# Optimization experiments

Measured on AMD Instinct MI355X. Metric: run time of the kernel, lower is better.

Reference implementation:

```python
import jax, jax.numpy as jnp
import numpy as np

B, T, C = 4, 1024, 768
H, HS = 12, 64           # num_heads, head_size
VD = 2 * HS              # value dim per head


def setup_inputs() -> dict:
    key = jax.random.key(0)
    ks = jax.random.split(key, 16)
    s = 0.02
    inp = {
        "x": jax.random.normal(ks[0], (B, T, C), jnp.float32),
        "Wq1": jax.random.normal(ks[1], (H, C, HS), jnp.float32) * s,
        "Wk1": jax.random.normal(ks[2], (H, C, HS), jnp.float32) * s,
        "Wq2": jax.random.normal(ks[3], (H, C, HS), jnp.float32) * s,
        "Wk2": jax.random.normal(ks[4], (H, C, HS), jnp.float32) * s,
        "Wv": jax.random.normal(ks[5], (H, C, VD), jnp.float32) * s,
        "lq1": jax.random.normal(ks[6], (H, HS), jnp.float32) * 0.1,
        "lk1": jax.random.normal(ks[7], (H, HS), jnp.float32) * 0.1,
        "lq2": jax.random.normal(ks[8], (H, HS), jnp.float32) * 0.1,
        "lk2": jax.random.normal(ks[9], (H, HS), jnp.float32) * 0.1,
        "gn_w": jnp.ones((H * VD,), jnp.float32),
        "gn_b": jnp.zeros((H * VD,), jnp.float32),
        "Wp": jax.random.normal(ks[10], (C, H * VD), jnp.float32) * s,
        "bp": jnp.zeros((C,), jnp.float32),
        "layer_idx": 3,
    }
    return inp


def _diff_attn(x, Wq1, Wk1, Wq2, Wk2, Wv, lq1, lk1, lq2, lk2,
               gn_w, gn_b, Wp, bp, layer_idx):
    Bc, Tc, _ = x.shape
    scale = 1.0 / jnp.sqrt(jnp.float32(HS))
    # per-head projections: [B,H,T,HS]
    q1 = jnp.einsum('btc,hcd->bhtd', x, Wq1)
    k1 = jnp.einsum('btc,hcd->bhtd', x, Wk1)
    q2 = jnp.einsum('btc,hcd->bhtd', x, Wq2)
    k2 = jnp.einsum('btc,hcd->bhtd', x, Wk2)
    v = jnp.einsum('btc,hce->bhte', x, Wv)           # [B,H,T,2HS]
    mask = jnp.tril(jnp.ones((Tc, Tc), bool))         # causal
    neg = jnp.float32(-jnp.inf)
    a1 = jnp.einsum('bhtd,bhsd->bhts', q1, k1) * scale
    a2 = jnp.einsum('bhtd,bhsd->bhts', q2, k2) * scale
    a1 = jax.nn.softmax(jnp.where(mask, a1, neg), axis=-1)
    a2 = jax.nn.softmax(jnp.where(mask, a2, neg), axis=-1)
    # dynamic lambda init, per get_lambda
    li = jnp.float32(layer_idx)
    dyn = 0.8 - 0.6 * jnp.exp(-0.3 * (li - 1.0))
    lam = jnp.mean(jnp.exp(lq1 * lk1) - jnp.exp(lq2 * lk2) + dyn, axis=-1)  # [H]
    diff = a1 - lam[None, :, None, None] * a2
    out = jnp.einsum('bhts,bhse->bhte', diff, v)      # [B,H,T,2HS]
    out = out.transpose(0, 2, 1, 3).reshape(Bc, Tc, H * VD)
    # GroupLayerNorm == full layernorm over last dim (unbiased=False var)
    mu = out.mean(-1, keepdims=True)
    var = jnp.mean((out - mu) ** 2, axis=-1, keepdims=True)
    out = (out - mu) / jnp.sqrt(var + 1e-5) * gn_w + gn_b
    out = out * 0.2  # (1 - lambda_init_buffer=0.8), buffer never updated
    return out @ Wp.T + bp


def reference(x, Wq1, Wk1, Wq2, Wk2, Wv, lq1, lk1, lq2, lk2,
              gn_w, gn_b, Wp, bp, layer_idx):
    return _diff_attn(x, Wq1, Wk1, Wq2, Wk2, Wv, lq1, lk1, lq2, lk2,
                      gn_w, gn_b, Wp, bp, layer_idx)
```

## Files before the change

### kernel.cpp

```cpp
#include <hip/hip_runtime.h>
#include <hip/hip_bf16.h>

#define Bc   4
#define Tc   1024
#define Cc   768
#define Hc   12
#define HSc  64
#define VDc  128
#define NQKV 4608
#define YLD  3072
#define NROWS 4096
#define HVD  1536

#define Q1OFF 0
#define K1OFF 768
#define Q2OFF 1536
#define K2OFF 2304

typedef __bf16 bf16x8 __attribute__((ext_vector_type(8)));
typedef float f32x4 __attribute__((ext_vector_type(4)));
typedef unsigned int u32x4 __attribute__((ext_vector_type(4)));

#define EXP2SCALE 0.18033688011112042f

static __device__ __forceinline__ float bf2f(unsigned short s) {
    return __uint_as_float(((unsigned int)s) << 16);
}
static __device__ __forceinline__ unsigned short f2bf(float f) {
    unsigned int u = __float_as_uint(f);
    unsigned int r = (u + 0x7FFFu + ((u >> 16) & 1u)) >> 16;
    return (unsigned short)r;
}
static __device__ __forceinline__ unsigned int pack2bf(float lo, float hi) {
    unsigned int a = (__float_as_uint(lo) + 0x8000u) >> 16;
    unsigned int b = (__float_as_uint(hi) + 0x8000u) & 0xFFFF0000u;
    return a | b;
}
static __device__ __forceinline__ float fast_exp2(float x) {
    float r;
    asm("v_exp_f32 %0, %1" : "=v"(r) : "v"(x));
    return r;
}

static __device__ __forceinline__ void load16_lds(const void* g, void* l) {
    __builtin_amdgcn_global_load_lds(
        (const __attribute__((address_space(1))) void*)g,
        (__attribute__((address_space(3))) void*)l, 16, 0, 0);
}

__global__ __launch_bounds__(256) void cast_bf16(
    const float* __restrict__ src, unsigned short* __restrict__ dst)
{
    int i = blockIdx.x * 256 + threadIdx.x;
    float4 v = *(const float4*)(src + (size_t)i * 4);
    ushort4 u;
    u.x = f2bf(v.x); u.y = f2bf(v.y); u.z = f2bf(v.z); u.w = f2bf(v.w);
    *(ushort4*)(dst + (size_t)i * 4) = u;
}

__global__ __launch_bounds__(256) void trans_w(
    const float* __restrict__ Wq1, const float* __restrict__ Wk1,
    const float* __restrict__ Wq2, const float* __restrict__ Wk2,
    const float* __restrict__ Wv, unsigned short* __restrict__ WcatT)
{
    __shared__ float tile[64][65];
    int tid = threadIdx.x;
    int t = blockIdx.x;
    int kt = t % 12, nt = t / 12;
    int k0 = kt * 64, n0 = nt * 64;
    const float* src;
    int stride;
    if (n0 < 3072) {
        int which = n0 / 768, m = n0 - which * 768, h = m >> 6;
        const float* W = (which == 0) ? Wq1 : (which == 1) ? Wk1 : (which == 2) ? Wq2 : Wk2;
        src = W + ((size_t)h * 768 + k0) * 64;
        stride = 64;
    } else {
        int rel = n0 - 3072, h = rel >> 7, e0 = rel & 127;
        src = Wv + ((size_t)h * 768 + k0) * 128 + e0;
        stride = 128;
    }
    for (int i = tid; i < 4096; i += 256) {
        int kl = i >> 6, dl = i & 63;
        tile[dl][kl] = src[(size_t)kl * stride + dl];
    }
    __syncthreads();
    for (int i = tid; i < 4096; i += 256) {
        int nl = i >> 6, kl = i & 63;
        WcatT[(size_t)(n0 + nl) * 768 + k0 + kl] = f2bf(tile[nl][kl]);
    }
}

__global__ __launch_bounds__(64) void lambda_kernel(
    const float* __restrict__ lq1, const float* __restrict__ lk1,
    const float* __restrict__ lq2, const float* __restrict__ lk2,
    const int* __restrict__ layer_idx, float* __restrict__ lam)
{
    int h = blockIdx.x, l = threadIdx.x;
    float li = (float)layer_idx[0];
    float dyn = 0.8f - 0.6f * expf(-0.3f * (li - 1.0f));
    int i = h * HSc + l;
    float v = expf(lq1[i] * lk1[i]) - expf(lq2[i] * lk2[i]) + dyn;
    #pragma unroll
    for (int off = 32; off; off >>= 1) v += __shfl_xor(v, off);
    if (l == 0) lam[h] = v * (1.0f / 64.0f);
}

template<int TN, int KD, int LDC, bool OUT_BIAS, bool SPLITV>
__global__ __launch_bounds__(256) void gemm_mfma(
    const unsigned short* __restrict__ A, const unsigned short* __restrict__ Bt,
    unsigned short* __restrict__ Cb, float* __restrict__ Cf,
    const float* __restrict__ bias, unsigned short* __restrict__ VtOut)
{
    constexpr int BN = TN * 32;
    constexpr int JB = TN / 2;
    __shared__ unsigned short As[128 * 64];
    __shared__ unsigned short Bs[BN * 64];
    int tid = threadIdx.x, lane = tid & 63, w = tid >> 6;
    int wm = w >> 1, wn = w & 1;
    int m0 = blockIdx.y * 128, n0 = blockIdx.x * BN;

    int lr = lane >> 2, lq = lane & 3;
    const unsigned short* gA[2];
    const unsigned short* gB[JB];
    #pragma unroll
    for (int j = 0; j < 2; ++j) {
        int row = w * 32 + j * 16 + lr;
        int qg = lq ^ ((row >> 1) & 3);
        gA[j] = A + (size_t)(m0 + row) * KD + qg * 8;
    }
    #pragma unroll
    for (int j = 0; j < JB; ++j) {
        int row = w * (JB * 16) + j * 16 + lr;
        int qg = lq ^ ((row >> 1) & 3);
        gB[j] = Bt + (size_t)(n0 + row) * KD + qg * 8;
    }

    int rr = lane & 15, qd = lane >> 4;
    const unsigned short* aAddr[4];
    const unsigned short* bAddr[TN];
    #pragma unroll
    for (int i = 0; i < 4; ++i) {
        int row = wm * 64 + i * 16 + rr;
        int qs = qd ^ ((row >> 1) & 3);
        aAddr[i] = As + row * 32 + qs * 8;
    }
    #pragma unroll
    for (int t = 0; t < TN; ++t) {
        int row = wn * (TN * 16) + t * 16 + rr;
        int qs = qd ^ ((row >> 1) & 3);
        bAddr[t] = Bs + row * 32 + qs * 8;
    }

    f32x4 acc[4][TN];
    #pragma unroll
    for (int i = 0; i < 4; ++i)
        #pragma unroll
        for (int t = 0; t < TN; ++t) acc[i][t] = {0.f, 0.f, 0.f, 0.f};

    for (int k = 0; k < KD / 64; ++k) {
        __syncthreads();
        load16_lds(gA[0], As + (w * 2 + 0) * 512);
        load16_lds(gA[1], As + (w * 2 + 1) * 512);
        load16_lds(gA[0] + 32, As + 4096 + (w * 2 + 0) * 512);
        load16_lds(gA[1] + 32, As + 4096 + (w * 2 + 1) * 512);
        #pragma unroll
        for (int j = 0; j < JB; ++j) {
            load16_lds(gB[j], Bs + (w * JB + j) * 512);
            load16_lds(gB[j] + 32, Bs + BN * 32 + (w * JB + j) * 512);
        }
        gA[0] += 64; gA[1] += 64;
        #pragma unroll
        for (int j = 0; j < JB; ++j) gB[j] += 64;
        __syncthreads();

        bf16x8 af0[4], af1[4], bf0[TN], bf1[TN];
        #pragma unroll
        for (int i = 0; i < 4; ++i) {
            af0[i] = *(const bf16x8*)aAddr[i];
            af1[i] = *(const bf16x8*)(aAddr[i] + 4096);
        }
        #pragma unroll
        for (int t = 0; t < TN; ++t) {
            bf0[t] = *(const bf16x8*)bAddr[t];
            bf1[t] = *(const bf16x8*)(bAddr[t] + BN * 32);
        }
        #pragma unroll
        for (int i = 0; i < 4; ++i)
            #pragma unroll
            for (int t = 0; t < TN; ++t) {
                acc[i][t] = __builtin_amdgcn_mfma_f32_16x16x32_bf16(af0[i], bf0[t], acc[i][t], 0, 0, 0);
                acc[i][t] = __builtin_amdgcn_mfma_f32_16x16x32_bf16(af1[i], bf1[t], acc[i][t], 0, 0, 0);
            }
    }

    #pragma unroll
    for (int t = 0; t < TN; ++t) {
        int col = n0 + wn * (TN * 16) + t * 16 + rr;
        if (SPLITV && col >= 3072) {
            int rel = col - 3072, hh = rel >> 7, e = rel & 127;
            #pragma unroll
            for (int i = 0; i < 4; ++i) {
                int row0 = m0 + wm * 64 + i * 16 + qd * 4;
                int b = row0 >> 10, tt = row0 & 1023;
                ushort4 pk;
                pk.x = f2bf(acc[i][t][0]); pk.y = f2bf(acc[i][t][1]);
                pk.z = f2bf(acc[i][t][2]); pk.w = f2bf(acc[i][t][3]);
                *(ushort4*)&VtOut[(size_t)((b * Hc + hh) * 128 + e) * 1024 + tt] = pk;
            }
        } else {
            float bv = OUT_BIAS ? bias[col] : 0.f;
            #pragma unroll
            for (int i = 0; i < 4; ++i) {
                #pragma unroll
                for (int r = 0; r < 4; ++r) {
                    int row = m0 + wm * 64 + i * 16 + qd * 4 + r;
                    if (OUT_BIAS)
                        Cf[(size_t)row * LDC + col] = acc[i][t][r] + bv;
                    else
                        Cb[(size_t)row * LDC + col] = f2bf(acc[i][t][r]);
                }
            }
        }
    }
}

__global__ __launch_bounds__(256) void diff_attn_mfma(
    const unsigned short* __restrict__ Y, const unsigned short* __restrict__ Vt,
    const float* __restrict__ lam_buf, unsigned short* __restrict__ attn)
{
    __shared__ __align__(16) unsigned short KVring[2 * 16384];

    int bh = blockIdx.x;
    int b = bh / Hc, h = bh - b * Hc;
    int g = 15 - (int)blockIdx.y;
    int tid = threadIdx.x, lane = tid & 63, wv = tid >> 6;
    int cl = lane & 15, qd = lane >> 4;
    float lamv = lam_buf[h];
    size_t rowbase = (size_t)(b * Tc) * YLD;
    const int hq = h * HSc;
    const unsigned short* VtB = Vt + ((size_t)bh << 17);
    const f32x4 zero4 = {0.f, 0.f, 0.f, 0.f};

    int sub = wv & 1;
    int off8[8];
    int dstoff;
    if (wv < 2) {
        int ksrow = lane >> 3;
        int ksch  = (lane & 7) ^ ksrow;
        #pragma unroll
        for (int j = 0; j < 8; ++j) {
            int moff = (j < 4) ? K1OFF : K2OFF;
            off8[j] = ((j & 3) * 8 + ksrow) * YLD + moff + hq + ksch * 8;
        }
        dstoff = 0;
    } else {
        int vsel = lane >> 2;
        int vsch = (lane & 3) ^ ((vsel >> 1) & 3);
        #pragma unroll
        for (int s = 0; s < 8; ++s)
            off8[s] = (s * 16 + vsel) * 1024 + vsch * 8;
        dstoff = 8192;
    }

    auto stage = [&](int i, int slot) {
        int kt = 2 * i + sub;
        char* base = (char*)KVring + slot * 32768 + sub * 16384 + dstoff;
        const unsigned short* g0 = (wv < 2)
            ? (Y + rowbase + (size_t)(kt * 32) * YLD)
            : (VtB + kt * 32);
        #pragma unroll
        for (int j = 0; j < 8; ++j)
            load16_lds(g0 + off8[j], base + j * 1024);
    };

    int kfo[2][4], vfo[8];
    #pragma unroll
    for (int c = 0; c < 2; ++c) {
        int row = c * 16 + cl;
        #pragma unroll
        for (int j = 0; j < 4; ++j)
            kfo[c][j] = (j >> 1) * 4096 + row * 128 +
                        ((((j & 1) * 4 + qd) ^ (row & 7)) << 4);
    }
    #pragma unroll
    for (int ec = 0; ec < 8; ++ec) {
        int e = ec * 16 + cl;
        vfo[ec] = 8192 + e * 64 + ((qd ^ ((e >> 1) & 3)) << 4);
    }

    int idxA = ((32 * (qd & 1)) + cl) * 4;
    int idxB = idxA + 64;
    bool loHalf = (qd < 2);

    int qrow = g * 64 + wv * 16;

    stage(0, 0);

    size_t qoff = rowbase + (size_t)(qrow + cl) * YLD;
    bf16x8 q1a = *(const bf16x8*)(Y + qoff + Q1OFF + hq + qd * 8);
    bf16x8 q1b = *(const bf16x8*)(Y + qoff + Q1OFF + hq + 32 + qd * 8);
    bf16x8 q2a = *(const bf16x8*)(Y + qoff + Q2OFF + hq + qd * 8);
    bf16x8 q2b = *(const bf16x8*)(Y + qoff + Q2OFF + hq + 32 + qd * 8);

    f32x4 O1[8], O2[8];
    #pragma unroll
    for (int ec = 0; ec < 8; ++ec) { O1[ec] = zero4; O2[ec] = zero4; }
    float l1s = 0.f, l2s = 0.f;

    auto transform = [&](f32x4 S1[2], f32x4 S2[2], int kt,
                         bf16x8& pa1o, bf16x8& pa2o) {
        if (kt * 32 + 31 > qrow) {
            #pragma unroll
            for (int c = 0; c < 2; ++c) {
                int lim = qrow + cl - kt * 32 - c * 16 - qd * 4;
                #pragma unroll
                for (int r = 0; r < 4; ++r) {
                    if (r > lim) { S1[c][r] = -1e30f; S2[c][r] = -1e30f; }
                }
            }
        }
        float p1v[2][4], p2v[2][4];
        #pragma unroll
        for (int c = 0; c < 2; ++c) {
            #pragma unroll
            for (int r = 0; r < 4; ++r) {
                p1v[c][r] = fast_exp2(S1[c][r] * EXP2SCALE);
                p2v[c][r] = fast_exp2(S2[c][r] * EXP2SCALE);
                l1s += p1v[c][r];
                l2s += p2v[c][r];
            }
        }
        unsigned int s1m[2][2], s2m[2][2];
        #pragma unroll
        for (int c = 0; c < 2; ++c) {
            s1m[c][0] = pack2bf(p1v[c][0], p1v[c][1]);
            s1m[c][1] = pack2bf(p1v[c][2], p1v[c][3]);
            s2m[c][0] = pack2bf(p2v[c][0], p2v[c][1]);
            s2m[c][1] = pack2bf(p2v[c][2], p2v[c][3]);
        }
        u32x4 U1, U2;
        {
            int a00 = __builtin_amdgcn_ds_bpermute(idxA, (int)s1m[0][0]);
            int a10 = __builtin_amdgcn_ds_bpermute(idxA, (int)s1m[1][0]);
            int a01 = __builtin_amdgcn_ds_bpermute(idxA, (int)s1m[0][1]);
            int a11 = __builtin_amdgcn_ds_bpermute(idxA, (int)s1m[1][1]);
            int b00 = __builtin_amdgcn_ds_bpermute(idxB, (int)s1m[0][0]);
            int b10 = __builtin_amdgcn_ds_bpermute(idxB, (int)s1m[1][0]);
            int b01 = __builtin_amdgcn_ds_bpermute(idxB, (int)s1m[0][1]);
            int b11 = __builtin_amdgcn_ds_bpermute(idxB, (int)s1m[1][1]);
            U1[0] = (unsigned)(loHalf ? a00 : a10);
            U1[1] = (unsigned)(loHalf ? a01 : a11);
            U1[2] = (unsigned)(loHalf ? b00 : b10);
            U1[3] = (unsigned)(loHalf ? b01 : b11);
        }
        {
            int a00 = __builtin_amdgcn_ds_bpermute(idxA, (int)s2m[0][0]);
            int a10 = __builtin_amdgcn_ds_bpermute(idxA, (int)s2m[1][0]);
            int a01 = __builtin_amdgcn_ds_bpermute(idxA, (int)s2m[0][1]);
            int a11 = __builtin_amdgcn_ds_bpermute(idxA, (int)s2m[1][1]);
            int b00 = __builtin_amdgcn_ds_bpermute(idxB, (int)s2m[0][0]);
            int b10 = __builtin_amdgcn_ds_bpermute(idxB, (int)s2m[1][0]);
            int b01 = __builtin_amdgcn_ds_bpermute(idxB, (int)s2m[0][1]);
            int b11 = __builtin_amdgcn_ds_bpermute(idxB, (int)s2m[1][1]);
            U2[0] = (unsigned)(loHalf ? a00 : a10);
            U2[1] = (unsigned)(loHalf ? a01 : a11);
            U2[2] = (unsigned)(loHalf ? b00 : b10);
            U2[3] = (unsigned)(loHalf ? b01 : b11);
        }
        pa1o = __builtin_bit_cast(bf16x8, U1);
        pa2o = __builtin_bit_cast(bf16x8, U2);
    };

    int NI = g + 1;
    for (int i = 0; i < NI; ++i) {
        asm volatile("s_waitcnt vmcnt(0)\n\ts_barrier" ::: "memory");
        const char* kbA = (const char*)KVring + (i & 1) * 32768;
        const char* kbB = kbA + 16384;
        if (i + 1 < NI) stage(i + 1, (i + 1) & 1);

        bf16x8 kfA[2][4], kfB[2][4];
        #pragma unroll
        for (int c = 0; c < 2; ++c)
            #pragma unroll
            for (int j = 0; j < 4; ++j) {
                kfA[c][j] = *(const bf16x8*)(kbA + kfo[c][j]);
                kfB[c][j] = *(const bf16x8*)(kbB + kfo[c][j]);
            }
        bf16x8 vfA[8];
        #pragma unroll
        for (int ec = 0; ec < 8; ++ec)
            vfA[ec] = *(const bf16x8*)(kbA + vfo[ec]);

        f32x4 S1A[2], S2A[2], S1B[2], S2B[2];
        #pragma unroll
        for (int c = 0; c < 2; ++c) {
            S1A[c] = zero4; S2A[c] = zero4; S1B[c] = zero4; S2B[c] = zero4;
        }
        #pragma unroll
        for (int c = 0; c < 2; ++c) {
            S1A[c] = __builtin_amdgcn_mfma_f32_16x16x32_bf16(kfA[c][0], q1a, S1A[c], 0, 0, 0);
            S1A[c] = __builtin_amdgcn_mfma_f32_16x16x32_bf16(kfA[c][1], q1b, S1A[c], 0, 0, 0);
            S2A[c] = __builtin_amdgcn_mfma_f32_16x16x32_bf16(kfA[c][2], q2a, S2A[c], 0, 0, 0);
            S2A[c] = __builtin_amdgcn_mfma_f32_16x16x32_bf16(kfA[c][3], q2b, S2A[c], 0, 0, 0);
            S1B[c] = __builtin_amdgcn_mfma_f32_16x16x32_bf16(kfB[c][0], q1a, S1B[c], 0, 0, 0);
            S1B[c] = __builtin_amdgcn_mfma_f32_16x16x32_bf16(kfB[c][1], q1b, S1B[c], 0, 0, 0);
            S2B[c] = __builtin_amdgcn_mfma_f32_16x16x32_bf16(kfB[c][2], q2a, S2B[c], 0, 0, 0);
            S2B[c] = __builtin_amdgcn_mfma_f32_16x16x32_bf16(kfB[c][3], q2b, S2B[c], 0, 0, 0);
        }

        bf16x8 pa1A, pa2A, pa1B, pa2B;
        transform(S1A, S2A, 2 * i, pa1A, pa2A);
        bf16x8 vfB[8];
        #pragma unroll
        for (int ec = 0; ec < 8; ++ec)
            vfB[ec] = *(const bf16x8*)(kbB + vfo[ec]);
        transform(S1B, S2B, 2 * i + 1, pa1B, pa2B);

        #pragma unroll
        for (int ec = 0; ec < 8; ++ec) {
            O1[ec] = __builtin_amdgcn_mfma_f32_16x16x32_bf16(pa1A, vfA[ec], O1[ec], 0, 0, 0);
            O2[ec] = __builtin_amdgcn_mfma_f32_16x16x32_bf16(pa2A, vfA[ec], O2[ec], 0, 0, 0);
        }
        #pragma unroll
        for (int ec = 0; ec < 8; ++ec) {
            O1[ec] = __builtin_amdgcn_mfma_f32_16x16x32_bf16(pa1B, vfB[ec], O1[ec], 0, 0, 0);
            O2[ec] = __builtin_amdgcn_mfma_f32_16x16x32_bf16(pa2B, vfB[ec], O2[ec], 0, 0, 0);
        }
    }

    l1s += __shfl_xor(l1s, 16); l1s += __shfl_xor(l1s, 32);
    l2s += __shfl_xor(l2s, 16); l2s += __shfl_xor(l2s, 32);
    float w1[4], w2[4];
    #pragma unroll
    for (int r = 0; r < 4; ++r) {
        float d1 = __shfl(l1s, qd * 4 + r);
        float d2 = __shfl(l2s, qd * 4 + r);
        w1[r] = 1.0f / d1;
        w2[r] = lamv / d2;
    }
    #pragma unroll
    for (int ec = 0; ec < 8; ++ec) {
        #pragma unroll
        for (int r = 0; r < 4; ++r) {
            size_t row = (size_t)(b * Tc + qrow + qd * 4 + r);
            attn[row * HVD + h * VDc + ec * 16 + cl] =
                f2bf(O1[ec][r] * w1[r] - O2[ec][r] * w2[r]);
        }
    }
}

__global__ __launch_bounds__(128) void ln_inplace(
    unsigned short* __restrict__ attn,
    const float* __restrict__ gnw, const float* __restrict__ gnb)
{
    int row = blockIdx.x, tid = threadIdx.x;
    unsigned short* p = attn + (size_t)row * HVD;
    float v[12];
    float s = 0.f, sq = 0.f;
    #pragma unroll
    for (int j = 0; j < 3; ++j) {
        int g = tid + j * 128;
        ushort4 u = *(const ushort4*)(p + g * 4);
        float x0 = bf2f(u.x), x1 = bf2f(u.y), x2 = bf2f(u.z), x3 = bf2f(u.w);
        v[j * 4 + 0] = x0; v[j * 4 + 1] = x1; v[j * 4 + 2] = x2; v[j * 4 + 3] = x3;
        s += x0 + x1 + x2 + x3;
        sq = fmaf(x0, x0, sq); sq = fmaf(x1, x1, sq);
        sq = fmaf(x2, x2, sq); sq = fmaf(x3, x3, sq);
    }
    #pragma unroll
    for (int off = 32; off; off >>= 1) { s += __shfl_xor(s, off); sq += __shfl_xor(sq, off); }
    __shared__ float ss[2], sqs[2];
    if ((tid & 63) == 0) { ss[tid >> 6] = s; sqs[tid >> 6] = sq; }
    __syncthreads();
    float S = ss[0] + ss[1], Q = sqs[0] + sqs[1];
    float mu = S * (1.0f / HVD);
    float rstd = rsqrtf(Q * (1.0f / HVD) - mu * mu + 1e-5f);
    #pragma unroll
    for (int j = 0; j < 3; ++j) {
        int g = tid + j * 128;
        float4 gw = *(const float4*)(gnw + g * 4);
        float4 gb = *(const float4*)(gnb + g * 4);
        ushort4 o;
        o.x = f2bf(((v[j * 4 + 0] - mu) * rstd * gw.x + gb.x) * 0.2f);
        o.y = f2bf(((v[j * 4 + 1] - mu) * rstd * gw.y + gb.y) * 0.2f);
        o.z = f2bf(((v[j * 4 + 2] - mu) * rstd * gw.z + gb.z) * 0.2f);
        o.w = f2bf(((v[j * 4 + 3] - mu) * rstd * gw.w + gb.w) * 0.2f);
        *(ushort4*)(p + g * 4) = o;
    }
}

extern "C" void kernel_launch(void* const* d_in, const int* in_sizes, int n_in,
                              void* d_out, int out_size, void* d_ws, size_t ws_size,
                              hipStream_t stream)
{
    const float* x   = (const float*)d_in[0];
    const float* Wq1 = (const float*)d_in[1];
    const float* Wk1 = (const float*)d_in[2];
    const float* Wq2 = (const float*)d_in[3];
    const float* Wk2 = (const float*)d_in[4];
    const float* Wv  = (const float*)d_in[5];
    const float* lq1 = (const float*)d_in[6];
    const float* lk1 = (const float*)d_in[7];
    const float* lq2 = (const float*)d_in[8];
    const float* lk2 = (const float*)d_in[9];
    const float* gnw = (const float*)d_in[10];
    const float* gnb = (const float*)d_in[11];
    const float* Wp  = (const float*)d_in[12];
    const float* bp  = (const float*)d_in[13];
    const int*   lidx = (const int*)d_in[14];
    float* out = (float*)d_out;

    char* w = (char*)d_ws;
    unsigned short* WcatT = (unsigned short*)(w);
    unsigned short* Xb    = (unsigned short*)(w + 7077888);
    unsigned short* Y     = (unsigned short*)(w + 13369344);
    unsigned short* VtW   = (unsigned short*)(w + 38535168);
    unsigned short* attn  = (unsigned short*)(w + 51118080);
    unsigned short* Wpb   = (unsigned short*)(w + 63700992);
    float* lam            = (float*)(w + 66060288);

    cast_bf16<<<dim3(NROWS * Cc / 1024), 256, 0, stream>>>(x, Xb);
    cast_bf16<<<dim3(Cc * HVD / 1024), 256, 0, stream>>>(Wp, Wpb);
    trans_w<<<dim3(72 * 12), 256, 0, stream>>>(Wq1, Wk1, Wq2, Wk2, Wv, WcatT);
    lambda_kernel<<<dim3(Hc), 64, 0, stream>>>(lq1, lk1, lq2, lk2, lidx, lam);
    gemm_mfma<4, 768, YLD, false, true><<<dim3(NQKV / 128, NROWS / 128), 256, 0, stream>>>(
        Xb, WcatT, Y, nullptr, nullptr, VtW);
    diff_attn_mfma<<<dim3(Bc * Hc, 16), 256, 0, stream>>>(Y, VtW, lam, attn);
    ln_inplace<<<dim3(NROWS), 128, 0, stream>>>(attn, gnw, gnb);
    gemm_mfma<2, HVD, Cc, true, false><<<dim3(Cc / 64, NROWS / 128), 256, 0, stream>>>(
        attn, Wpb, nullptr, out, bp, nullptr);
}
```

Measured before the change: 240.5 us.

## Merge prep kernels and remap GEMM blocks for XCD-local L2 reuse

Folds the two fp32-to-bf16 casts and the lambda computation into a single prep kernel, removing two launches. Both GEMMs switch to a 1D grid with a block-index swizzle: the low 3 bits pick an XCD, and each XCD is given 4 consecutive M tiles, so tiles that share A rows stay in one XCD's L2. This aims to cut launch overhead and L2 misses. It depends on blocks being dispatched round-robin across the 8 XCDs, and the index arithmetic only matches the current 32 M tiles.

```diff
diff --git a/kernel.cpp b/kernel.cpp
--- a/kernel.cpp
+++ b/kernel.cpp
@@ -48,14 +48,37 @@
         (__attribute__((address_space(3))) void*)l, 16, 0, 0);
 }
 
-__global__ __launch_bounds__(256) void cast_bf16(
-    const float* __restrict__ src, unsigned short* __restrict__ dst)
+__global__ __launch_bounds__(256) void prep(
+    const float* __restrict__ x, const float* __restrict__ Wp,
+    const float* __restrict__ lq1, const float* __restrict__ lk1,
+    const float* __restrict__ lq2, const float* __restrict__ lk2,
+    const int* __restrict__ layer_idx,
+    unsigned short* __restrict__ Xb, unsigned short* __restrict__ Wpb,
+    float* __restrict__ lam)
 {
-    int i = blockIdx.x * 256 + threadIdx.x;
-    float4 v = *(const float4*)(src + (size_t)i * 4);
-    ushort4 u;
-    u.x = f2bf(v.x); u.y = f2bf(v.y); u.z = f2bf(v.z); u.w = f2bf(v.w);
-    *(ushort4*)(dst + (size_t)i * 4) = u;
+    int bid = blockIdx.x, tid = threadIdx.x;
+    if (bid < 3072) {
+        size_t i = (size_t)bid * 256 + tid;
+        float4 v = *(const float4*)(x + i * 4);
+        ushort4 u;
+        u.x = f2bf(v.x); u.y = f2bf(v.y); u.z = f2bf(v.z); u.w = f2bf(v.w);
+        *(ushort4*)(Xb + i * 4) = u;
+    } else if (bid < 4224) {
+        size_t i = (size_t)(bid - 3072) * 256 + tid;
+        float4 v = *(const float4*)(Wp + i * 4);
+        ushort4 u;
+        u.x = f2bf(v.x); u.y = f2bf(v.y); u.z = f2bf(v.z); u.w = f2bf(v.w);
+        *(ushort4*)(Wpb + i * 4) = u;
+    } else if (tid < 64) {
+        int h = bid - 4224, l = tid;
+        float li = (float)layer_idx[0];
+        float dyn = 0.8f - 0.6f * expf(-0.3f * (li - 1.0f));
+        int i = h * HSc + l;
+        float v = expf(lq1[i] * lk1[i]) - expf(lq2[i] * lk2[i]) + dyn;
+        #pragma unroll
+        for (int off = 32; off; off >>= 1) v += __shfl_xor(v, off);
+        if (l == 0) lam[h] = v * (1.0f / 64.0f);
+    }
 }
 
 __global__ __launch_bounds__(256) void trans_w(
@@ -91,21 +114,6 @@
     }
 }
 
-__global__ __launch_bounds__(64) void lambda_kernel(
-    const float* __restrict__ lq1, const float* __restrict__ lk1,
-    const float* __restrict__ lq2, const float* __restrict__ lk2,
-    const int* __restrict__ layer_idx, float* __restrict__ lam)
-{
-    int h = blockIdx.x, l = threadIdx.x;
-    float li = (float)layer_idx[0];
-    float dyn = 0.8f - 0.6f * expf(-0.3f * (li - 1.0f));
-    int i = h * HSc + l;
-    float v = expf(lq1[i] * lk1[i]) - expf(lq2[i] * lk2[i]) + dyn;
-    #pragma unroll
-    for (int off = 32; off; off >>= 1) v += __shfl_xor(v, off);
-    if (l == 0) lam[h] = v * (1.0f / 64.0f);
-}
-
 template<int TN, int KD, int LDC, bool OUT_BIAS, bool SPLITV>
 __global__ __launch_bounds__(256) void gemm_mfma(
     const unsigned short* __restrict__ A, const unsigned short* __restrict__ Bt,
@@ -118,7 +126,14 @@
     __shared__ unsigned short Bs[BN * 64];
     int tid = threadIdx.x, lane = tid & 63, w = tid >> 6;
     int wm = w >> 1, wn = w & 1;
-    int m0 = blockIdx.y * 128, n0 = blockIdx.x * BN;
+
+    int bid = blockIdx.x;
+    int xcd = bid & 7;
+    int idx = bid >> 3;
+    int mi  = idx & 3;
+    int ni  = idx >> 2;
+    int m0 = (xcd * 4 + mi) * 128;
+    int n0 = ni * BN;
 
     int lr = lane >> 2, lq = lane & 3;
     const unsigned short* gA[2];
@@ -520,14 +535,13 @@
     unsigned short* Wpb   = (unsigned short*)(w + 63700992);
     float* lam            = (float*)(w + 66060288);
 
-    cast_bf16<<<dim3(NROWS * Cc / 1024), 256, 0, stream>>>(x, Xb);
-    cast_bf16<<<dim3(Cc * HVD / 1024), 256, 0, stream>>>(Wp, Wpb);
+    prep<<<dim3(4236), 256, 0, stream>>>(x, Wp, lq1, lk1, lq2, lk2, lidx,
+                                         Xb, Wpb, lam);
     trans_w<<<dim3(72 * 12), 256, 0, stream>>>(Wq1, Wk1, Wq2, Wk2, Wv, WcatT);
-    lambda_kernel<<<dim3(Hc), 64, 0, stream>>>(lq1, lk1, lq2, lk2, lidx, lam);
-    gemm_mfma<4, 768, YLD, false, true><<<dim3(NQKV / 128, NROWS / 128), 256, 0, stream>>>(
+    gemm_mfma<4, 768, YLD, false, true><<<dim3(1152), 256, 0, stream>>>(
         Xb, WcatT, Y, nullptr, nullptr, VtW);
     diff_attn_mfma<<<dim3(Bc * Hc, 16), 256, 0, stream>>>(Y, VtW, lam, attn);
     ln_inplace<<<dim3(NROWS), 128, 0, stream>>>(attn, gnw, gnb);
-    gemm_mfma<2, HVD, Cc, true, false><<<dim3(Cc / 64, NROWS / 128), 256, 0, stream>>>(
+    gemm_mfma<2, HVD, Cc, true, false><<<dim3(384), 256, 0, stream>>>(
         attn, Wpb, nullptr, out, bp, nullptr);
 }
```

After: 235.6 us. 2.0% less time.
